# Kernel optimization log

Measured on AMD Instinct MI355X. Metric: run time of the kernel, lower is better.

The kernel has to match this reference:

```python
import jax, jax.numpy as jnp
import numpy as np

NUM_CLOTHES = 50000
FEAT_DIM = 256
BATCH = 1024
MOMENTUM = 0.0
SCALE = 16.0
EPSILON = 0.1


def setup_inputs() -> dict:
    key = jax.random.key(0)
    k1, k2, k3, k4 = jax.random.split(key, 4)
    inputs = jax.random.normal(k1, (BATCH, FEAT_DIM), dtype=jnp.float32)
    feature_memory = jax.random.normal(k2, (NUM_CLOTHES, FEAT_DIM), dtype=jnp.float32)
    targets = jax.random.randint(k3, (BATCH,), 0, NUM_CLOTHES, dtype=jnp.int64)
    # binary positive mask; guarantee the identity (own-clothes) column is positive
    positive_mask = (jax.random.uniform(k4, (BATCH, NUM_CLOTHES)) < 0.01).astype(jnp.float32)
    positive_mask = positive_mask.at[jnp.arange(BATCH), targets].set(1.0)
    return {"inputs": inputs, "feature_memory": feature_memory,
            "positive_mask": positive_mask, "targets": targets}


def _l2_normalize(x, axis=-1):
    # matches F.normalize(p=2): divide by max(||x||, 1e-12)
    n = jnp.sqrt(jnp.sum(x * x, axis=axis, keepdims=True))
    return x / jnp.maximum(n, 1e-12)


def reference(inputs, feature_memory, positive_mask, targets):
    B = inputs.shape[0]
    # ---- memory update: scatter-mean of detached features per clothes label ----
    feats = jax.lax.stop_gradient(inputs)
    sums = jax.ops.segment_sum(feats, targets, num_segments=NUM_CLOTHES)      # [C, D]
    counts = jax.ops.segment_sum(jnp.ones((B,), feats.dtype), targets,
                                 num_segments=NUM_CLOTHES)                     # [C]
    mean = sums / jnp.maximum(counts, 1.0)[:, None]
    present = (counts > 0)[:, None]
    memory = jnp.where(present,
                       MOMENTUM * feature_memory + (1.0 - MOMENTUM) * mean,
                       feature_memory)                                         # [C, D]
    memory = jax.lax.stop_gradient(memory)
    # ---- similarities against memory bank ----
    inputs_norm = _l2_normalize(inputs)
    memory_norm = _l2_normalize(memory)
    similarities = jnp.einsum('bd,cd->bc', inputs_norm, memory_norm) * SCALE   # [B, C]
    # ---- masked log-sum-exp loss ----
    negative_mask = 1.0 - positive_mask
    mask_identity = jax.nn.one_hot(targets, NUM_CLOTHES, dtype=similarities.dtype)
    exp_logits = jnp.exp(similarities)
    neg_sum = jnp.sum(exp_logits * negative_mask, axis=1, keepdims=True)       # [B, 1]
    log_prob = similarities - jnp.log(neg_sum + exp_logits)
    pos_count = jnp.sum(positive_mask, axis=1, keepdims=True)
    mask = (1.0 - EPSILON) * mask_identity + (EPSILON / pos_count) * positive_mask
    loss = jnp.mean(jnp.sum(-mask * log_prob, axis=1))
    return loss
```

## Files before the change

### kernel.cpp

```cpp
#include <hip/hip_runtime.h>
#include <hip/hip_bf16.h>
#include <stdint.h>

#define NCLOTHES 50000
#define CPAD     50048
#define NWORDS   782
#define NCB2     782
#define FDIM     256
#define NBATCH   1024
#define SCALEF   16.0f
#define EPSW     0.1f
#define SLOTS    8

typedef __attribute__((ext_vector_type(8))) short short8;
typedef __attribute__((ext_vector_type(4))) float f32x4;

__device__ __forceinline__ void gload_lds16(const void* gsrc, void* ldst) {
    __builtin_amdgcn_global_load_lds(
        (const __attribute__((address_space(1))) void*)gsrc,
        (__attribute__((address_space(3))) void*)ldst, 16, 0, 0);
}

__global__ void anorm_kernel(const float* __restrict__ in, __hip_bfloat16* __restrict__ A) {
    int b = blockIdx.x, t = threadIdx.x;
    float x = in[b * FDIM + t];
    float ss = x * x;
    #pragma unroll
    for (int o = 32; o > 0; o >>= 1) ss += __shfl_xor(ss, o);
    __shared__ float sh[4];
    if ((t & 63) == 0) sh[t >> 6] = ss;
    __syncthreads();
    float tot = sh[0] + sh[1] + sh[2] + sh[3];
    float r = SCALEF / fmaxf(sqrtf(tot), 1e-12f);
    A[b * FDIM + t] = __float2bfloat16(x * r);
}

__global__ __launch_bounds__(256)
void bnorm_all(const float* __restrict__ fm, __hip_bfloat16* __restrict__ Bm) {
    const int nw = (gridDim.x * 256) >> 6;
    int w = (blockIdx.x * 256 + threadIdx.x) >> 6;
    int lane = threadIdx.x & 63;
    for (int row = w; row < CPAD; row += nw) {
        __hip_bfloat16 h[4];
        if (row >= NCLOTHES) {
            h[0] = h[1] = h[2] = h[3] = __float2bfloat16(0.f);
        } else {
            f32x4 v = *(const f32x4*)(fm + (size_t)row * FDIM + lane * 4);
            float ss = v.x * v.x + v.y * v.y + v.z * v.z + v.w * v.w;
            #pragma unroll
            for (int o = 32; o > 0; o >>= 1) ss += __shfl_xor(ss, o);
            float r = 1.f / fmaxf(sqrtf(ss), 1e-12f);
            h[0] = __float2bfloat16(v.x * r);
            h[1] = __float2bfloat16(v.y * r);
            h[2] = __float2bfloat16(v.z * r);
            h[3] = __float2bfloat16(v.w * r);
        }
        *(ushort4*)(Bm + (size_t)row * FDIM + lane * 4) = *(const ushort4*)h;
    }
}

__global__ void bnorm_present(const float* __restrict__ in, const int* __restrict__ tg,
                              __hip_bfloat16* __restrict__ Bm) {
    int b = blockIdx.x, t = threadIdx.x;
    __shared__ int stg[NBATCH];
    #pragma unroll
    for (int j = 0; j < 4; ++j) stg[t + j * 256] = tg[t + j * 256];
    __syncthreads();
    int c = stg[b];
    bool dup = false;
    #pragma unroll
    for (int j = 0; j < 4; ++j) {
        int i = t + j * 256;
        if (i < b && stg[i] == c) dup = true;
    }
    if (__syncthreads_or(dup)) return;
    __shared__ int mlist[64];
    __shared__ int mcount;
    if (t == 0) mcount = 0;
    __syncthreads();
    #pragma unroll
    for (int j = 0; j < 4; ++j) {
        int i = t + j * 256;
        if (stg[i] == c) { int p = atomicAdd(&mcount, 1); if (p < 64) mlist[p] = i; }
    }
    __syncthreads();
    int n = mcount;
    float v = 0.f;
    for (int i = 0; i < n; ++i) v += in[mlist[i] * FDIM + t];
    v /= (float)n;
    float ss = v * v;
    #pragma unroll
    for (int o = 32; o > 0; o >>= 1) ss += __shfl_xor(ss, o);
    __shared__ float sh[4];
    if ((t & 63) == 0) sh[t >> 6] = ss;
    __syncthreads();
    float tot = sh[0] + sh[1] + sh[2] + sh[3];
    float r = 1.0f / fmaxf(sqrtf(tot), 1e-12f);
    Bm[(size_t)c * FDIM + t] = __float2bfloat16(v * r);
}

__global__ __launch_bounds__(256)
void pack_kernel(const float* __restrict__ pm, unsigned long long* __restrict__ maskw) {
    const int row = blockIdx.x;
    const int half = blockIdx.y;
    const int wave = threadIdx.x >> 6;
    const int lane = threadIdx.x & 63;
    const float* prow = pm + (size_t)row * NCLOTHES;
    unsigned long long* wrow = maskw + (size_t)row * NWORDS;
    for (int chunk = half * 98 + wave; chunk < half * 98 + 98; chunk += 4) {
        int base = chunk * 256;
        unsigned long long b0, b1, b2, b3;
        {
            int c0 = base + lane;
            float v0 = (c0 < NCLOTHES) ? prow[c0] : 0.f;
            float v1 = (c0 + 64 < NCLOTHES) ? prow[c0 + 64] : 0.f;
            float v2 = (c0 + 128 < NCLOTHES) ? prow[c0 + 128] : 0.f;
            float v3 = (c0 + 192 < NCLOTHES) ? prow[c0 + 192] : 0.f;
            b0 = __ballot(v0 >= 0.5f);
            b1 = __ballot(v1 >= 0.5f);
            b2 = __ballot(v2 >= 0.5f);
            b3 = __ballot(v3 >= 0.5f);
        }
        if (lane < 4) {
            int wi = chunk * 4 + lane;
            unsigned long long w = (lane == 0) ? b0 : (lane == 1) ? b1 : (lane == 2) ? b2 : b3;
            if (wi < NWORDS) wrow[wi] = w;
        }
    }
}

#define BM 128
#define BN 128
#define BK 32
#define NKSTEP (FDIM / BK)

__global__ __launch_bounds__(256, 4)
void gemm_kernel(const __hip_bfloat16* __restrict__ A, const __hip_bfloat16* __restrict__ Bm,
                 const unsigned long long* __restrict__ maskw,
                 float* __restrict__ partial_ns,
                 float* __restrict__ sbuf)
{
    __shared__ alignas(16) __hip_bfloat16 As[2][BM * BK];
    __shared__ alignas(16) __hip_bfloat16 Bs[2][BM * BK];

    const int t = threadIdx.x;
    const int bx = blockIdx.x;
    const int bn0 = bx * BN;
    const int bm0 = blockIdx.y * BM;

    const int lane = t & 63;
    const int wave = t >> 6;
    const int wr = wave >> 1, wc = wave & 1;
    const int lrow = lane & 15, lq = lane >> 4;

    const int sr = t >> 2;
    const int sk = (t & 3) * 8;

    f32x4 acc[4][4];
    #pragma unroll
    for (int m = 0; m < 4; ++m)
        #pragma unroll
        for (int n = 0; n < 4; ++n) acc[m][n] = (f32x4)0.f;

    {
        const __hip_bfloat16* ag = A + (size_t)(bm0 + sr) * FDIM + sk;
        const __hip_bfloat16* bg = Bm + (size_t)(bn0 + sr) * FDIM + sk;
        gload_lds16(ag,             (void*)&As[0][t * 8]);
        gload_lds16(ag + 64 * FDIM, (void*)&As[0][2048 + t * 8]);
        gload_lds16(bg,             (void*)&Bs[0][t * 8]);
        gload_lds16(bg + 64 * FDIM, (void*)&Bs[0][2048 + t * 8]);
    }

    for (int ks = 0; ks < NKSTEP; ++ks) {
        __syncthreads();
        int cur = ks & 1;
        if (ks + 1 < NKSTEP) {
            int nxt = cur ^ 1;
            int k0 = (ks + 1) * BK;
            const __hip_bfloat16* ag = A + (size_t)(bm0 + sr) * FDIM + k0 + sk;
            const __hip_bfloat16* bg = Bm + (size_t)(bn0 + sr) * FDIM + k0 + sk;
            gload_lds16(ag,             (void*)&As[nxt][t * 8]);
            gload_lds16(ag + 64 * FDIM, (void*)&As[nxt][2048 + t * 8]);
            gload_lds16(bg,             (void*)&Bs[nxt][t * 8]);
            gload_lds16(bg + 64 * FDIM, (void*)&Bs[nxt][2048 + t * 8]);
        }
        short8 af[4], bf[4];
        #pragma unroll
        for (int m = 0; m < 4; ++m)
            af[m] = *(const short8*)&As[cur][(wr * 64 + m * 16 + lrow) * BK + lq * 8];
        #pragma unroll
        for (int n = 0; n < 4; ++n)
            bf[n] = *(const short8*)&Bs[cur][(wc * 64 + n * 16 + lrow) * BK + lq * 8];
        #pragma unroll
        for (int m = 0; m < 4; ++m)
            #pragma unroll
            for (int n = 0; n < 4; ++n)
                acc[m][n] = __builtin_amdgcn_mfma_f32_16x16x32_bf16(af[m], bf[n], acc[m][n], 0, 0, 0);
    }

    const int rowbase = bm0 + wr * 64;
    const int colbase = bn0 + wc * 64;
    const int cb2 = bx * 2 + wc;

    unsigned long long mwv[4][4];
    #pragma unroll
    for (int m = 0; m < 4; ++m)
        #pragma unroll
        for (int r = 0; r < 4; ++r) {
            int grow = rowbase + m * 16 + lq * 4 + r;
            mwv[m][r] = maskw[(size_t)grow * NWORDS + cb2];
        }

    #pragma unroll
    for (int m = 0; m < 4; ++m) {
        #pragma unroll
        for (int r = 0; r < 4; ++r) {
            const int grow = rowbase + m * 16 + lq * 4 + r;
            const unsigned long long mw = mwv[m][r];
            float pneg = 0.f;
            #pragma unroll
            for (int n = 0; n < 4; ++n) {
                const int p = n * 16 + lrow;
                bool vld = (colbase + p) < NCLOTHES;
                bool pos = (mw >> p) & 1ull;
                pneg += (vld && !pos) ? __expf(acc[m][n][r]) : 0.f;
            }
            pneg += __shfl_xor(pneg, 1);
            pneg += __shfl_xor(pneg, 2);
            pneg += __shfl_xor(pneg, 4);
            pneg += __shfl_xor(pneg, 8);
            const size_t base = ((size_t)cb2 * NBATCH + grow);
            #pragma unroll
            for (int n = 0; n < 4; ++n) {
                const int p = n * 16 + lrow;
                if ((mw >> p) & 1ull) {
                    int pre = __popcll(mw & ((1ull << p) - 1ull));
                    if (pre < SLOTS) sbuf[base * SLOTS + pre] = acc[m][n][r];
                }
            }
            if (lrow == 0) partial_ns[base] = pneg;
        }
    }
}

__global__ void finish_kernel(const float* __restrict__ partial_ns,
                              const unsigned long long* __restrict__ maskw,
                              const float* __restrict__ sbuf,
                              const int* __restrict__ tg, float* __restrict__ loss_rows) {
    int b = blockIdx.x, t = threadIdx.x;
    int tgt = tg[b];
    const int cbt = tgt >> 6, bitp = tgt & 63;

    float ns = 0.f;
    for (int cb = t; cb < NCB2; cb += 256) ns += partial_ns[(size_t)cb * NBATCH + b];
    #pragma unroll
    for (int o = 32; o > 0; o >>= 1) ns += __shfl_xor(ns, o);
    __shared__ float shn[4];
    if ((t & 63) == 0) shn[t >> 6] = ns;
    __syncthreads();
    ns = shn[0] + shn[1] + shn[2] + shn[3];

    float slp = 0.f, idlp = 0.f;
    int np = 0;
    for (int cb = t; cb < NCB2; cb += 256) {
        unsigned long long mw = maskw[(size_t)b * NWORDS + cb];
        int k = __popcll(mw);
        np += k;
        int kk = k < SLOTS ? k : SLOTS;
        const float* sp = sbuf + ((size_t)cb * NBATCH + b) * SLOTS;
        for (int i = 0; i < kk; ++i) {
            float s = sp[i];
            slp += s - __logf(ns + __expf(s));
        }
        if (cb == cbt) {
            int idslot = __popcll(mw & ((1ull << bitp) - 1ull));
            if (idslot < SLOTS) {
                float s = sp[idslot];
                idlp = s - __logf(ns + __expf(s));
            }
        }
    }
    #pragma unroll
    for (int o = 32; o > 0; o >>= 1) {
        slp += __shfl_xor(slp, o);
        idlp += __shfl_xor(idlp, o);
        np += __shfl_xor(np, o);
    }
    __shared__ float sh1[4], sh2[4];
    __shared__ int shp[4];
    if ((t & 63) == 0) { sh1[t >> 6] = slp; sh2[t >> 6] = idlp; shp[t >> 6] = np; }
    __syncthreads();
    if (t == 0) {
        float s_all = sh1[0] + sh1[1] + sh1[2] + sh1[3];
        float i_all = sh2[0] + sh2[1] + sh2[2] + sh2[3];
        int np_all = shp[0] + shp[1] + shp[2] + shp[3];
        loss_rows[b] = -((1.0f - EPSW) * i_all + (EPSW / (float)np_all) * s_all);
    }
}

__global__ void reduce_kernel(const float* __restrict__ lr, float* __restrict__ out) {
    int t = threadIdx.x;
    float s = lr[t] + lr[t + 256] + lr[t + 512] + lr[t + 768];
    #pragma unroll
    for (int o = 32; o > 0; o >>= 1) s += __shfl_xor(s, o);
    __shared__ float sh[4];
    if ((t & 63) == 0) sh[t >> 6] = s;
    __syncthreads();
    if (t == 0) out[0] = (sh[0] + sh[1] + sh[2] + sh[3]) * (1.0f / NBATCH);
}

extern "C" void kernel_launch(void* const* d_in, const int* in_sizes, int n_in,
                              void* d_out, int out_size, void* d_ws, size_t ws_size,
                              hipStream_t stream) {
    const float* inputs  = (const float*)d_in[0];
    const float* fm      = (const float*)d_in[1];
    const float* pmask   = (const float*)d_in[2];
    const int*   targets = (const int*)d_in[3];
    float* out = (float*)d_out;

    char* ws = (char*)d_ws;
    size_t off = 0;
    __hip_bfloat16* A = (__hip_bfloat16*)(ws + off);  off += (size_t)NBATCH * FDIM * 2;
    __hip_bfloat16* Bm = (__hip_bfloat16*)(ws + off); off += (size_t)CPAD * FDIM * 2;
    off = (off + 255) & ~(size_t)255;
    unsigned long long* maskw = (unsigned long long*)(ws + off); off += (size_t)NBATCH * NWORDS * 8;
    float* partial_ns = (float*)(ws + off);        off += (size_t)NCB2 * NBATCH * 4;
    float* sbuf = (float*)(ws + off);              off += (size_t)NCB2 * NBATCH * SLOTS * 4;
    off = (off + 255) & ~(size_t)255;
    float* loss_rows = (float*)(ws + off);         off += 4096;

    anorm_kernel<<<NBATCH, 256, 0, stream>>>(inputs, A);
    bnorm_all<<<2048, 256, 0, stream>>>(fm, Bm);
    bnorm_present<<<NBATCH, 256, 0, stream>>>(inputs, targets, Bm);
    pack_kernel<<<dim3(NBATCH, 2), 256, 0, stream>>>(pmask, maskw);
    gemm_kernel<<<dim3(CPAD / BN, NBATCH / BM), 256, 0, stream>>>(A, Bm, maskw, partial_ns, sbuf);
    finish_kernel<<<NBATCH, 256, 0, stream>>>(partial_ns, maskw, sbuf, targets, loss_rows);
    reduce_kernel<<<1, 256, 0, stream>>>(loss_rows, out);
}
```

Measured before the change: 469.1 us.

## Merge prep kernels, transpose sbuf to row-major, split negative-sum reduction

```diff
diff --git a/kernel.cpp b/kernel.cpp
--- a/kernel.cpp
+++ b/kernel.cpp
@@ -21,41 +21,72 @@
         (__attribute__((address_space(3))) void*)ldst, 16, 0, 0);
 }
 
-__global__ void anorm_kernel(const float* __restrict__ in, __hip_bfloat16* __restrict__ A) {
-    int b = blockIdx.x, t = threadIdx.x;
-    float x = in[b * FDIM + t];
-    float ss = x * x;
-    #pragma unroll
-    for (int o = 32; o > 0; o >>= 1) ss += __shfl_xor(ss, o);
-    __shared__ float sh[4];
-    if ((t & 63) == 0) sh[t >> 6] = ss;
-    __syncthreads();
-    float tot = sh[0] + sh[1] + sh[2] + sh[3];
-    float r = SCALEF / fmaxf(sqrtf(tot), 1e-12f);
-    A[b * FDIM + t] = __float2bfloat16(x * r);
-}
-
 __global__ __launch_bounds__(256)
-void bnorm_all(const float* __restrict__ fm, __hip_bfloat16* __restrict__ Bm) {
-    const int nw = (gridDim.x * 256) >> 6;
-    int w = (blockIdx.x * 256 + threadIdx.x) >> 6;
-    int lane = threadIdx.x & 63;
-    for (int row = w; row < CPAD; row += nw) {
-        __hip_bfloat16 h[4];
-        if (row >= NCLOTHES) {
-            h[0] = h[1] = h[2] = h[3] = __float2bfloat16(0.f);
-        } else {
-            f32x4 v = *(const f32x4*)(fm + (size_t)row * FDIM + lane * 4);
-            float ss = v.x * v.x + v.y * v.y + v.z * v.z + v.w * v.w;
-            #pragma unroll
-            for (int o = 32; o > 0; o >>= 1) ss += __shfl_xor(ss, o);
-            float r = 1.f / fmaxf(sqrtf(ss), 1e-12f);
-            h[0] = __float2bfloat16(v.x * r);
-            h[1] = __float2bfloat16(v.y * r);
-            h[2] = __float2bfloat16(v.z * r);
-            h[3] = __float2bfloat16(v.w * r);
-        }
-        *(ushort4*)(Bm + (size_t)row * FDIM + lane * 4) = *(const ushort4*)h;
+void prep1_kernel(const float* __restrict__ in, const float* __restrict__ fm,
+                  const float* __restrict__ pm,
+                  __hip_bfloat16* __restrict__ A, __hip_bfloat16* __restrict__ Bm,
+                  unsigned long long* __restrict__ maskw) {
+    const int blk = blockIdx.x;
+    const int t = threadIdx.x;
+
+    if (blk < 1024) {
+        int b = blk;
+        float x = in[b * FDIM + t];
+        float ss = x * x;
+        #pragma unroll
+        for (int o = 32; o > 0; o >>= 1) ss += __shfl_xor(ss, o);
+        __shared__ float sh[4];
+        if ((t & 63) == 0) sh[t >> 6] = ss;
+        __syncthreads();
+        float tot = sh[0] + sh[1] + sh[2] + sh[3];
+        float r = SCALEF / fmaxf(sqrtf(tot), 1e-12f);
+        A[b * FDIM + t] = __float2bfloat16(x * r);
+    } else if (blk < 3072) {
+        int p = blk - 1024;
+        const int row = p >> 1;
+        const int half = p & 1;
+        const int wave = t >> 6;
+        const int lane = t & 63;
+        const float* prow = pm + (size_t)row * NCLOTHES;
+        unsigned long long* wrow = maskw + (size_t)row * NWORDS;
+        for (int chunk = half * 98 + wave; chunk < half * 98 + 98; chunk += 4) {
+            int base = chunk * 256;
+            int c0 = base + lane;
+            float v0 = (c0 < NCLOTHES) ? prow[c0] : 0.f;
+            float v1 = (c0 + 64 < NCLOTHES) ? prow[c0 + 64] : 0.f;
+            float v2 = (c0 + 128 < NCLOTHES) ? prow[c0 + 128] : 0.f;
+            float v3 = (c0 + 192 < NCLOTHES) ? prow[c0 + 192] : 0.f;
+            unsigned long long b0 = __ballot(v0 >= 0.5f);
+            unsigned long long b1 = __ballot(v1 >= 0.5f);
+            unsigned long long b2 = __ballot(v2 >= 0.5f);
+            unsigned long long b3 = __ballot(v3 >= 0.5f);
+            if (lane < 4) {
+                int wi = chunk * 4 + lane;
+                unsigned long long w = (lane == 0) ? b0 : (lane == 1) ? b1 : (lane == 2) ? b2 : b3;
+                if (wi < NWORDS) wrow[wi] = w;
+            }
+        }
+    } else {
+        const int nw = 2048 * 4;
+        int w = ((blk - 3072) * 256 + t) >> 6;
+        int lane = t & 63;
+        for (int row = w; row < CPAD; row += nw) {
+            __hip_bfloat16 h[4];
+            if (row >= NCLOTHES) {
+                h[0] = h[1] = h[2] = h[3] = __float2bfloat16(0.f);
+            } else {
+                f32x4 v = *(const f32x4*)(fm + (size_t)row * FDIM + lane * 4);
+                float ss = v.x * v.x + v.y * v.y + v.z * v.z + v.w * v.w;
+                #pragma unroll
+                for (int o = 32; o > 0; o >>= 1) ss += __shfl_xor(ss, o);
+                float r = 1.f / fmaxf(sqrtf(ss), 1e-12f);
+                h[0] = __float2bfloat16(v.x * r);
+                h[1] = __float2bfloat16(v.y * r);
+                h[2] = __float2bfloat16(v.z * r);
+                h[3] = __float2bfloat16(v.w * r);
+            }
+            *(ushort4*)(Bm + (size_t)row * FDIM + lane * 4) = *(const ushort4*)h;
+        }
     }
 }
 
@@ -97,36 +128,6 @@
     float tot = sh[0] + sh[1] + sh[2] + sh[3];
     float r = 1.0f / fmaxf(sqrtf(tot), 1e-12f);
     Bm[(size_t)c * FDIM + t] = __float2bfloat16(v * r);
-}
-
-__global__ __launch_bounds__(256)
-void pack_kernel(const float* __restrict__ pm, unsigned long long* __restrict__ maskw) {
-    const int row = blockIdx.x;
-    const int half = blockIdx.y;
-    const int wave = threadIdx.x >> 6;
-    const int lane = threadIdx.x & 63;
-    const float* prow = pm + (size_t)row * NCLOTHES;
-    unsigned long long* wrow = maskw + (size_t)row * NWORDS;
-    for (int chunk = half * 98 + wave; chunk < half * 98 + 98; chunk += 4) {
-        int base = chunk * 256;
-        unsigned long long b0, b1, b2, b3;
-        {
-            int c0 = base + lane;
-            float v0 = (c0 < NCLOTHES) ? prow[c0] : 0.f;
-            float v1 = (c0 + 64 < NCLOTHES) ? prow[c0 + 64] : 0.f;
-            float v2 = (c0 + 128 < NCLOTHES) ? prow[c0 + 128] : 0.f;
-            float v3 = (c0 + 192 < NCLOTHES) ? prow[c0 + 192] : 0.f;
-            b0 = __ballot(v0 >= 0.5f);
-            b1 = __ballot(v1 >= 0.5f);
-            b2 = __ballot(v2 >= 0.5f);
-            b3 = __ballot(v3 >= 0.5f);
-        }
-        if (lane < 4) {
-            int wi = chunk * 4 + lane;
-            unsigned long long w = (lane == 0) ? b0 : (lane == 1) ? b1 : (lane == 2) ? b2 : b3;
-            if (wi < NWORDS) wrow[wi] = w;
-        }
-    }
 }
 
 #define BM 128
@@ -202,21 +203,12 @@
     const int colbase = bn0 + wc * 64;
     const int cb2 = bx * 2 + wc;
 
-    unsigned long long mwv[4][4];
-    #pragma unroll
-    for (int m = 0; m < 4; ++m)
-        #pragma unroll
-        for (int r = 0; r < 4; ++r) {
-            int grow = rowbase + m * 16 + lq * 4 + r;
-            mwv[m][r] = maskw[(size_t)grow * NWORDS + cb2];
-        }
-
     #pragma unroll
     for (int m = 0; m < 4; ++m) {
         #pragma unroll
         for (int r = 0; r < 4; ++r) {
             const int grow = rowbase + m * 16 + lq * 4 + r;
-            const unsigned long long mw = mwv[m][r];
+            const unsigned long long mw = maskw[(size_t)grow * NWORDS + cb2];
             float pneg = 0.f;
             #pragma unroll
             for (int n = 0; n < 4; ++n) {
@@ -229,54 +221,59 @@
             pneg += __shfl_xor(pneg, 2);
             pneg += __shfl_xor(pneg, 4);
             pneg += __shfl_xor(pneg, 8);
-            const size_t base = ((size_t)cb2 * NBATCH + grow);
+            const size_t srow = (size_t)grow * NCB2 + cb2;
             #pragma unroll
             for (int n = 0; n < 4; ++n) {
                 const int p = n * 16 + lrow;
                 if ((mw >> p) & 1ull) {
                     int pre = __popcll(mw & ((1ull << p) - 1ull));
-                    if (pre < SLOTS) sbuf[base * SLOTS + pre] = acc[m][n][r];
+                    if (pre < SLOTS) sbuf[srow * SLOTS + pre] = acc[m][n][r];
                 }
             }
-            if (lrow == 0) partial_ns[base] = pneg;
-        }
-    }
-}
-
-__global__ void finish_kernel(const float* __restrict__ partial_ns,
+            if (lrow == 0) partial_ns[(size_t)cb2 * NBATCH + grow] = pneg;
+        }
+    }
+}
+
+__global__ void nsum_kernel(const float* __restrict__ partial_ns, float* __restrict__ negsum) {
+    int b = blockIdx.x * 256 + threadIdx.x;
+    float s = 0.f;
+    #pragma unroll 8
+    for (int cb = 0; cb < NCB2; ++cb) s += partial_ns[(size_t)cb * NBATCH + b];
+    negsum[b] = s;
+}
+
+__global__ void finish_kernel(const float* __restrict__ negsum,
                               const unsigned long long* __restrict__ maskw,
                               const float* __restrict__ sbuf,
                               const int* __restrict__ tg, float* __restrict__ loss_rows) {
     int b = blockIdx.x, t = threadIdx.x;
     int tgt = tg[b];
     const int cbt = tgt >> 6, bitp = tgt & 63;
-
-    float ns = 0.f;
-    for (int cb = t; cb < NCB2; cb += 256) ns += partial_ns[(size_t)cb * NBATCH + b];
-    #pragma unroll
-    for (int o = 32; o > 0; o >>= 1) ns += __shfl_xor(ns, o);
-    __shared__ float shn[4];
-    if ((t & 63) == 0) shn[t >> 6] = ns;
-    __syncthreads();
-    ns = shn[0] + shn[1] + shn[2] + shn[3];
+    const float ns = negsum[b];
+
+    const unsigned long long* mrow = maskw + (size_t)b * NWORDS;
+    const float* srow = sbuf + (size_t)b * NCB2 * SLOTS;
 
     float slp = 0.f, idlp = 0.f;
     int np = 0;
     for (int cb = t; cb < NCB2; cb += 256) {
-        unsigned long long mw = maskw[(size_t)b * NWORDS + cb];
-        int k = __popcll(mw);
-        np += k;
-        int kk = k < SLOTS ? k : SLOTS;
-        const float* sp = sbuf + ((size_t)cb * NBATCH + b) * SLOTS;
-        for (int i = 0; i < kk; ++i) {
-            float s = sp[i];
-            slp += s - __logf(ns + __expf(s));
-        }
-        if (cb == cbt) {
-            int idslot = __popcll(mw & ((1ull << bitp) - 1ull));
-            if (idslot < SLOTS) {
-                float s = sp[idslot];
-                idlp = s - __logf(ns + __expf(s));
+        unsigned long long mw = mrow[cb];
+        if (mw) {
+            int k = __popcll(mw);
+            np += k;
+            int kk = k < SLOTS ? k : SLOTS;
+            const float* sp = srow + (size_t)cb * SLOTS;
+            for (int i = 0; i < kk; ++i) {
+                float s = sp[i];
+                slp += s - __logf(ns + __expf(s));
+            }
+            if (cb == cbt) {
+                int idslot = __popcll(mw & ((1ull << bitp) - 1ull));
+                if (idslot < SLOTS) {
+                    float s = sp[idslot];
+                    idlp = s - __logf(ns + __expf(s));
+                }
             }
         }
     }
@@ -325,15 +322,14 @@
     off = (off + 255) & ~(size_t)255;
     unsigned long long* maskw = (unsigned long long*)(ws + off); off += (size_t)NBATCH * NWORDS * 8;
     float* partial_ns = (float*)(ws + off);        off += (size_t)NCB2 * NBATCH * 4;
-    float* sbuf = (float*)(ws + off);              off += (size_t)NCB2 * NBATCH * SLOTS * 4;
-    off = (off + 255) & ~(size_t)255;
+    float* sbuf = (float*)(ws + off);              off += (size_t)NBATCH * NCB2 * SLOTS * 4;
+    float* negsum = (float*)(ws + off);            off += 4096;
     float* loss_rows = (float*)(ws + off);         off += 4096;
 
-    anorm_kernel<<<NBATCH, 256, 0, stream>>>(inputs, A);
-    bnorm_all<<<2048, 256, 0, stream>>>(fm, Bm);
+    prep1_kernel<<<5120, 256, 0, stream>>>(inputs, fm, pmask, A, Bm, maskw);
     bnorm_present<<<NBATCH, 256, 0, stream>>>(inputs, targets, Bm);
-    pack_kernel<<<dim3(NBATCH, 2), 256, 0, stream>>>(pmask, maskw);
     gemm_kernel<<<dim3(CPAD / BN, NBATCH / BM), 256, 0, stream>>>(A, Bm, maskw, partial_ns, sbuf);
-    finish_kernel<<<NBATCH, 256, 0, stream>>>(partial_ns, maskw, sbuf, targets, loss_rows);
+    nsum_kernel<<<4, 256, 0, stream>>>(partial_ns, negsum);
+    finish_kernel<<<NBATCH, 256, 0, stream>>>(negsum, maskw, sbuf, targets, loss_rows);
     reduce_kernel<<<1, 256, 0, stream>>>(loss_rows, out);
 }
```

Result: slower. 502.6 us (+7.1%).
